# Kernel optimization log

Measured on AMD Instinct MI355X. Metric: run time of the kernel, lower is better.

The kernel has to match this reference:

```python
import jax, jax.numpy as jnp
import numpy as np

# norse default LIFParameters
DT = 1e-3
TAU_SYN_INV = 200.0
TAU_MEM_INV = 100.0
V_LEAK = 0.0
V_TH = 1.0
V_RESET = 0.0


def heaviside(x):
    return (x > 0).astype(x.dtype)


def setup_inputs() -> dict:
    key = jax.random.key(0)
    ks = jax.random.split(key, 5)
    T, B, I, H, O = 14, 4096, 2048, 1024, 128
    x = (jax.random.uniform(ks[0], (T, B, I), dtype=jnp.float32) < 0.2).astype(jnp.float32)  # spike train
    w_in = jax.random.normal(ks[1], (H, I), dtype=jnp.float32) * (1.0 / np.sqrt(I))
    w_rec = jax.random.normal(ks[2], (H, H), dtype=jnp.float32) * (1.0 / np.sqrt(H))
    out_w = jax.random.normal(ks[3], (O, H), dtype=jnp.float32) * (1.0 / np.sqrt(H))
    out_b = jax.random.normal(ks[4], (O,), dtype=jnp.float32) * 0.01
    return {"x": x, "w_in": w_in, "w_rec": w_rec, "out_w": out_w, "out_b": out_b}


def reference(x, w_in, w_rec, out_w, out_b):
    T, B, _ = x.shape
    H = w_in.shape[0]
    z0 = jnp.zeros((B, H), dtype=x.dtype)
    v0 = jnp.full((B, H), V_LEAK, dtype=x.dtype)
    i0 = jnp.zeros((B, H), dtype=x.dtype)

    def step(carry, x_t):
        z, v, i = carry
        v_dec = v + DT * TAU_MEM_INV * ((V_LEAK - v) + i)   # membrane integration
        i_dec = i - DT * TAU_SYN_INV * i                    # synaptic decay
        z_new = heaviside(v_dec - V_TH)                     # spike
        v_new = (1.0 - z_new) * v_dec + z_new * V_RESET     # reset
        i_new = i_dec + x_t @ w_in.T + z @ w_rec.T          # input + recurrent current
        return (z_new, v_new, i_new), None

    (z_T, _, _), _ = jax.lax.scan(step, (z0, v0, i0), x)
    return z_T @ out_w.T + out_b
```

## Files before the change

kernel.cpp:

```cpp
#include <hip/hip_runtime.h>
#include <stdint.h>

#define T_STEPS 14
#define B_DIM   4096
#define I_DIM   2048
#define H_DIM   1024
#define O_DIM   128
#define K_TOT   3072
#define ZBYTES  ((size_t)B_DIM * H_DIM)

#define WSCALE_F 33554432.0f

typedef __bf16  bf16x8  __attribute__((ext_vector_type(8)));
typedef float   floatx4 __attribute__((ext_vector_type(4)));
typedef int     int4v   __attribute__((ext_vector_type(4)));
typedef int     int16v  __attribute__((ext_vector_type(16)));
typedef unsigned long long u64;

__device__ __forceinline__ uint16_t f2bf_rne(float f) {
    uint32_t u = __float_as_uint(f);
    u += 0x7fffu + ((u >> 16) & 1u);
    return (uint16_t)(u >> 16);
}
__device__ __forceinline__ float bf2f(uint16_t h) {
    return __uint_as_float(((uint32_t)h) << 16);
}

__device__ __forceinline__ void gload_lds16(const void* g, void* l) {
    __builtin_amdgcn_global_load_lds((__attribute__((address_space(1))) void*)g,
                                     (__attribute__((address_space(3))) void*)l, 16, 0, 0);
}


__global__ void split_w_kernel(const float* __restrict__ w_in, const float* __restrict__ w_rec,
                               int8_t* __restrict__ WB) {
    int idx = blockIdx.x * 256 + threadIdx.x;
    int h = idx / K_TOT;
    int k = idx - h * K_TOT;
    float w = (k < I_DIM) ? w_in[(size_t)h * I_DIM + k]
                          : w_rec[(size_t)h * H_DIM + (k - I_DIM)];
    int W  = __float2int_rn(w * WSCALE_F);
    int d0 = (int8_t)(W & 0xFF);
    int r1 = (W - d0) >> 8;
    int d1 = (int8_t)(r1 & 0xFF);
    int d2 = (r1 - d1) >> 8;
    int nt = h >> 5, n32 = h & 31;
    int ktw = k >> 7, k128 = k & 127;
    int kk = k128 >> 5, half = (k128 >> 4) & 1, j = k128 & 15;
    int lane = half * 32 + n32;
    size_t base = (size_t)(nt * 24 + ktw) * 12288 + kk * 1024 + lane * 16 + j;
    WB[base] = (int8_t)d0; WB[base + 4096] = (int8_t)d1; WB[base + 8192] = (int8_t)d2;
}

__global__ void split_ow_kernel(const float* __restrict__ out_w, uint16_t* __restrict__ OW3) {
    int idx = blockIdx.x * 256 + threadIdx.x;
    float w = out_w[idx];
    uint16_t hi = f2bf_rne(w);
    float r1 = w - bf2f(hi);
    uint16_t mid = f2bf_rne(r1);
    float r2 = r1 - bf2f(mid);
    uint16_t lo = f2bf_rne(r2);
    const size_t S = (size_t)O_DIM * H_DIM;
    OW3[idx] = hi; OW3[idx + S] = mid; OW3[idx + 2 * S] = lo;
}

__global__ void cvt_x_kernel(const float* __restrict__ x, int8_t* __restrict__ xb) {
    size_t gid = (size_t)blockIdx.x * 256 + threadIdx.x;
    int g = (int)(gid & 1023);
    size_t chunk = gid >> 10;
    int kt   = (int)(chunk & 15);
    int mIdx = (int)((chunk >> 4) & 31);
    int t    = (int)(chunk >> 9);
    int group = g >> 8, kk = (g >> 6) & 3, lane = g & 63;
    int half = lane >> 5, row32 = lane & 31;
    int b = mIdx * 128 + group * 32 + row32;
    int k = kt * 128 + kk * 32 + half * 16;
    const float4* src = (const float4*)(x + ((size_t)t * B_DIM + b) * I_DIM + k);
    union { int8_t bytes[16]; int4v v; } u;
#pragma unroll
    for (int q = 0; q < 4; ++q) {
        float4 f = src[q];
        u.bytes[q * 4 + 0] = (int8_t)(f.x > 0.5f);
        u.bytes[q * 4 + 1] = (int8_t)(f.y > 0.5f);
        u.bytes[q * 4 + 2] = (int8_t)(f.z > 0.5f);
        u.bytes[q * 4 + 3] = (int8_t)(f.w > 0.5f);
    }
    ((int4v*)xb)[gid] = u.v;
}

__global__ void zero_cnt_kernel(uint32_t* __restrict__ cnt) {
    __hip_atomic_store(&cnt[blockIdx.x * 256 + threadIdx.x], 0u,
                       __ATOMIC_RELAXED, __HIP_MEMORY_SCOPE_AGENT);
}

__device__ __forceinline__ void loadA(const int8_t* __restrict__ aP, int4v (&a)[4]) {
    a[0] = *(const int4v*)(aP);
    a[1] = *(const int4v*)(aP + 1024);
    a[2] = *(const int4v*)(aP + 2048);
    a[3] = *(const int4v*)(aP + 3072);
}

__device__ __forceinline__ void stage_b0(const int8_t* __restrict__ bChunk0,
                                         int8_t* sB0, int wave, int lane) {
    gload_lds16(bChunk0 + (size_t)wave * 1024 + lane * 16,       sB0 + wave * 1024);
    gload_lds16(bChunk0 + (size_t)(4 + wave) * 1024 + lane * 16, sB0 + (4 + wave) * 1024);
    gload_lds16(bChunk0 + (size_t)(8 + wave) * 1024 + lane * 16, sB0 + (8 + wave) * 1024);
}

__device__ __forceinline__ void lif_iter_p(const int8_t* __restrict__ aPn,
                                           const int8_t* __restrict__ bPn,
                                           const int8_t* cur, int8_t* nxt,
                                           int4v (&aC)[4], int4v (&aN)[4],
                                           int wave, int lane, bool stage_next,
                                           int16v (&acc)[3]) {
    if (stage_next) {
        loadA(aPn, aN);
        gload_lds16(bPn + (size_t)wave * 1024 + lane * 16,       nxt + wave * 1024);
        gload_lds16(bPn + (size_t)(4 + wave) * 1024 + lane * 16, nxt + (4 + wave) * 1024);
        gload_lds16(bPn + (size_t)(8 + wave) * 1024 + lane * 16, nxt + (8 + wave) * 1024);
        __builtin_amdgcn_sched_barrier(0);
        asm volatile("s_waitcnt vmcnt(7)" ::: "memory");
    } else {
        asm volatile("s_waitcnt vmcnt(0)" ::: "memory");
    }
    __builtin_amdgcn_s_barrier();
    __builtin_amdgcn_sched_barrier(0);
#pragma unroll
    for (int kk = 0; kk < 4; ++kk) {
#pragma unroll
        for (int s = 0; s < 3; ++s) {
            int4v bF = *(const int4v*)(cur + s * 4096 + kk * 1024 + lane * 16);
            acc[s] = __builtin_amdgcn_mfma_i32_32x32x32_i8(aC[kk], bF, acc[s], 0, 0, 0);
        }
    }
    asm volatile("s_waitcnt lgkmcnt(0)" ::: "memory");
    __builtin_amdgcn_s_barrier();
}

template<int NKT>
__device__ __forceinline__ void run_phase(const int8_t* __restrict__ aW,
                                          const int8_t* __restrict__ bC,
                                          int8_t* sB0, int8_t* sB1,
                                          int4v (&aA)[4], int4v (&aB)[4],
                                          int wave, int lane, int16v (&acc)[3]) {
#pragma unroll 1
    for (int kt = 0; kt + 2 < NKT; kt += 2) {
        lif_iter_p(aW + (size_t)(kt + 1) * 16384, bC + (size_t)(kt + 1) * 12288,
                   sB0, sB1, aA, aB, wave, lane, true, acc);
        lif_iter_p(aW + (size_t)(kt + 2) * 16384, bC + (size_t)(kt + 2) * 12288,
                   sB1, sB0, aB, aA, wave, lane, true, acc);
    }
    lif_iter_p(aW + (size_t)(NKT - 1) * 16384, bC + (size_t)(NKT - 1) * 12288,
               sB0, sB1, aA, aB, wave, lane, true, acc);
    lif_iter_p(nullptr, nullptr, sB1, sB0, aB, aA, wave, lane, false, acc);
}

__launch_bounds__(256, 4)
__global__ void lif_persist_kernel(const int8_t* __restrict__ Xall,
                                   const int8_t* __restrict__ WB,
                                   int8_t* __restrict__ ZS,
                                   uint16_t* __restrict__ Zbf,
                                   uint32_t* __restrict__ cnt) {
    __shared__ int8_t sB0[12288];
    __shared__ int8_t sB1[12288];
    __shared__ int8_t sZ[4096];

    const int tid  = threadIdx.x;
    const int wave = tid >> 6, lane = tid & 63;
    const int lane32 = lane & 31, hl = lane >> 5;

    const int bid = blockIdx.x;
    const int xs = bid & 7, q = bid >> 3;
    const int mIdx = (xs & 1) * 16 + (q & 15);
    const int nt   = (xs >> 1) * 8 + (q >> 4);

    const int mBase = mIdx * 128, nBase = nt * 32;
    const int8_t* wbStrip = WB + (size_t)nt * 24 * 12288;
    const int fragOff = wave * 4096 + lane * 16;

    float vmem[16], isyn[16];
#pragma unroll
    for (int r = 0; r < 16; ++r) { vmem[r] = 0.0f; isyn[r] = 0.0f; }

    int4v aA[4], aB[4];

    stage_b0(wbStrip, sB0, wave, lane);
    loadA(Xall + (size_t)mIdx * 16 * 16384 + fragOff, aA);

    for (int t = 0; t < T_STEPS; ++t) {
        int16v acc[3] = {};

        const int8_t* XtW = Xall + (size_t)t * ((size_t)B_DIM * I_DIM)
                          + (size_t)mIdx * 16 * 16384 + fragOff;
        run_phase<16>(XtW, wbStrip, sB0, sB1, aA, aB, wave, lane, acc);

        if (t > 0) {
            const int8_t* zbChunk = wbStrip + (size_t)16 * 12288;
            stage_b0(zbChunk, sB0, wave, lane);
            if (tid == 0) {
                const uint32_t* f = cnt + ((size_t)mIdx * 13 + (t - 1)) * 32;
                while (__hip_atomic_load((uint32_t*)f, __ATOMIC_RELAXED, __HIP_MEMORY_SCOPE_AGENT) < 32u)
                    __builtin_amdgcn_s_sleep(2);
            }
            __syncthreads();
            const int8_t* zW = ZS + (size_t)(t - 1) * ZBYTES + (size_t)mIdx * 8 * 16384 + fragOff;
            loadA(zW, aA);
            run_phase<8>(zW, zbChunk, sB0, sB1, aA, aB, wave, lane, acc);
        }

        if (t + 1 < T_STEPS) {
            stage_b0(wbStrip, sB0, wave, lane);
            loadA(Xall + (size_t)(t + 1) * ((size_t)B_DIM * I_DIM)
                  + (size_t)mIdx * 16 * 16384 + fragOff, aA);
        }

#pragma unroll
        for (int r = 0; r < 16; ++r) {
#pragma clang fp contract(off)
            float cur = (float)acc[2][r] * (1.0f / 512.0f)
                      + (float)acc[1][r] * (1.0f / 131072.0f)
                      + (float)acc[0][r] * (1.0f / 33554432.0f);
            int row = (r & 3) + 8 * (r >> 2) + 4 * hl;
            float v_dec = vmem[r] + 0.1f * ((0.0f - vmem[r]) + isyn[r]);
            float i_dec = isyn[r] - 0.2f * isyn[r];
            bool z = (v_dec > 1.0f);
            vmem[r] = z ? 0.0f : v_dec;
            isyn[r] = i_dec + cur;
            if (t == T_STEPS - 1) {
                int b = mBase + wave * 32 + row;
                int h = nBase + lane32;
                Zbf[(size_t)b * H_DIM + h] = z ? (uint16_t)0x3F80 : (uint16_t)0;
            } else {
                sZ[wave * 1024 + ((lane32 >> 4) * 32 + row) * 16 + (lane32 & 15)]
                    = z ? (int8_t)1 : (int8_t)0;
            }
        }

        if (t < T_STEPS - 1) {
            __syncthreads();
            const u64* sp = (const u64*)&sZ[tid * 16];
            u64 v0 = sp[0], v1 = sp[1];
            int8_t* dst = ZS + (size_t)t * ZBYTES + ((size_t)mIdx * 8 + (nt >> 2)) * 16384
                        + (tid >> 6) * 4096 + (nt & 3) * 1024 + (tid & 63) * 16;
            __hip_atomic_store((u64*)dst,       v0, __ATOMIC_RELAXED, __HIP_MEMORY_SCOPE_AGENT);
            __hip_atomic_store((u64*)(dst + 8), v1, __ATOMIC_RELAXED, __HIP_MEMORY_SCOPE_AGENT);
            __syncthreads();
            if (tid == 0)
                __hip_atomic_fetch_add(&cnt[((size_t)mIdx * 13 + t) * 32], 1u,
                                       __ATOMIC_RELAXED, __HIP_MEMORY_SCOPE_AGENT);
        }
    }
}

__launch_bounds__(256)
__global__ void out_gemm_kernel(const uint16_t* __restrict__ Zfin,
                                const uint16_t* __restrict__ OW3,
                                const float* __restrict__ out_b,
                                float* __restrict__ out) {
    __shared__ uint16_t sA[16 * 32];
    __shared__ uint16_t sB[3][128 * 32];

    const int tid  = threadIdx.x;
    const int wave = tid >> 6, lane = tid & 63;
    const int quad = lane >> 4, col = lane & 15;

    const int mBase = blockIdx.x * 16;

    floatx4 acc[2] = {};

    const int ldRow = lane >> 2;
    const int ldCol = (lane & 3) * 8;

    for (int kt = 0; kt < H_DIM / 32; ++kt) {
        const int kb = kt * 32;
        __syncthreads();
        if (wave == 0) {
            const uint16_t* g = Zfin + (size_t)(mBase + ldRow) * H_DIM + kb + ldCol;
            gload_lds16(g, &sA[0]);
        }
#pragma unroll
        for (int s = 0; s < 3; ++s) {
            const uint16_t* wsrc = OW3 + (size_t)s * O_DIM * H_DIM;
#pragma unroll
            for (int j = 0; j < 2; ++j) {
                const int rseg = j * 4 + wave;
                const uint16_t* g = wsrc + (size_t)(rseg * 16 + ldRow) * H_DIM + kb + ldCol;
                gload_lds16(g, &sB[s][rseg * 16 * 32]);
            }
        }
        __syncthreads();

        bf16x8 aF = *reinterpret_cast<const bf16x8*>(&sA[col * 32 + quad * 8]);
#pragma unroll
        for (int s = 0; s < 3; ++s) {
#pragma unroll
            for (int ni = 0; ni < 2; ++ni) {
                int row = wave * 32 + ni * 16 + col;
                bf16x8 bF = *reinterpret_cast<const bf16x8*>(&sB[s][row * 32 + quad * 8]);
                acc[ni] = __builtin_amdgcn_mfma_f32_16x16x32_bf16(aF, bF, acc[ni], 0, 0, 0);
            }
        }
    }

    {
#pragma clang fp contract(off)
#pragma unroll
        for (int ni = 0; ni < 2; ++ni)
#pragma unroll
            for (int r = 0; r < 4; ++r) {
                int b = mBase + quad * 4 + r;
                int h = wave * 32 + ni * 16 + col;
                out[(size_t)b * O_DIM + h] = acc[ni][r] + out_b[h];
            }
    }
}

extern "C" void kernel_launch(void* const* d_in, const int* in_sizes, int n_in,
                              void* d_out, int out_size, void* d_ws, size_t ws_size,
                              hipStream_t stream) {
    const float* x     = (const float*)d_in[0];
    const float* w_in  = (const float*)d_in[1];
    const float* w_rec = (const float*)d_in[2];
    const float* out_w = (const float*)d_in[3];
    const float* out_b = (const float*)d_in[4];
    float* out = (float*)d_out;

    char* ws = (char*)d_ws;
    size_t off = 0;
    int8_t*   WB   = (int8_t*)(ws + off);   off += (size_t)3 * H_DIM * K_TOT;
    uint16_t* OW3  = (uint16_t*)(ws + off); off += (size_t)3 * O_DIM * H_DIM * 2;
    int8_t*   Xall = (int8_t*)(ws + off);   off += (size_t)T_STEPS * B_DIM * I_DIM;
    uint16_t* Zbf  = (uint16_t*)(ws + off); off += (size_t)B_DIM * H_DIM * 2;
    int8_t*   ZS   = (int8_t*)(ws + off);   off += (size_t)13 * ZBYTES;
    uint32_t* CNT  = (uint32_t*)(ws + off); off += (size_t)32 * 13 * 32 * 4;

    split_w_kernel<<<(H_DIM * K_TOT) / 256, 256, 0, stream>>>(w_in, w_rec, WB);
    split_ow_kernel<<<(O_DIM * H_DIM) / 256, 256, 0, stream>>>(out_w, OW3);
    cvt_x_kernel<<<(int)(((size_t)T_STEPS * B_DIM * I_DIM / 16) / 256), 256, 0, stream>>>(x, Xall);
    zero_cnt_kernel<<<(32 * 13 * 32) / 256, 256, 0, stream>>>(CNT);

    lif_persist_kernel<<<dim3(1024), dim3(256), 0, stream>>>(Xall, WB, ZS, Zbf, CNT);

    out_gemm_kernel<<<B_DIM / 16, 256, 0, stream>>>(Zbf, OW3, out_b, out);
}
```

Before: 1.356 ms.

## Single-buffer A fragments, issue next A loads after MFMAs, raise MFMA priority, remap blocks

Replaces the double-buffered A register fragments with a single set that is reloaded right after the MFMA block finishes, which frees registers. The wait count drops because only the B LDS copies are outstanding at the wait. MFMA sections are wrapped with s_setprio to favour matrix work. The block-to-tile mapping also changes so neighbouring blocks share different M/N strips, which alters L2 reuse. In exchange, A loads are no longer hidden behind a full iteration of compute.

```diff
diff --git a/kernel.cpp b/kernel.cpp
--- a/kernel.cpp
+++ b/kernel.cpp
@@ -107,32 +107,35 @@
     gload_lds16(bChunk0 + (size_t)(8 + wave) * 1024 + lane * 16, sB0 + (8 + wave) * 1024);
 }
 
-__device__ __forceinline__ void lif_iter_p(const int8_t* __restrict__ aPn,
-                                           const int8_t* __restrict__ bPn,
-                                           const int8_t* cur, int8_t* nxt,
-                                           int4v (&aC)[4], int4v (&aN)[4],
-                                           int wave, int lane, bool stage_next,
-                                           int16v (&acc)[3]) {
+__device__ __forceinline__ void lif_iter(const int8_t* __restrict__ aPn,
+                                         const int8_t* __restrict__ bPn,
+                                         const int8_t* cur, int8_t* nxt,
+                                         int4v (&aA)[4],
+                                         int wave, int lane, bool stage_next,
+                                         int16v (&acc)[3]) {
     if (stage_next) {
-        loadA(aPn, aN);
         gload_lds16(bPn + (size_t)wave * 1024 + lane * 16,       nxt + wave * 1024);
         gload_lds16(bPn + (size_t)(4 + wave) * 1024 + lane * 16, nxt + (4 + wave) * 1024);
         gload_lds16(bPn + (size_t)(8 + wave) * 1024 + lane * 16, nxt + (8 + wave) * 1024);
         __builtin_amdgcn_sched_barrier(0);
-        asm volatile("s_waitcnt vmcnt(7)" ::: "memory");
+        asm volatile("s_waitcnt vmcnt(3)" ::: "memory");
     } else {
         asm volatile("s_waitcnt vmcnt(0)" ::: "memory");
     }
     __builtin_amdgcn_s_barrier();
     __builtin_amdgcn_sched_barrier(0);
+    __builtin_amdgcn_s_setprio(1);
 #pragma unroll
     for (int kk = 0; kk < 4; ++kk) {
 #pragma unroll
         for (int s = 0; s < 3; ++s) {
             int4v bF = *(const int4v*)(cur + s * 4096 + kk * 1024 + lane * 16);
-            acc[s] = __builtin_amdgcn_mfma_i32_32x32x32_i8(aC[kk], bF, acc[s], 0, 0, 0);
-        }
-    }
+            acc[s] = __builtin_amdgcn_mfma_i32_32x32x32_i8(aA[kk], bF, acc[s], 0, 0, 0);
+        }
+    }
+    __builtin_amdgcn_s_setprio(0);
+    __builtin_amdgcn_sched_barrier(0);
+    if (aPn) loadA(aPn, aA);
     asm volatile("s_waitcnt lgkmcnt(0)" ::: "memory");
     __builtin_amdgcn_s_barrier();
 }
@@ -141,18 +144,18 @@
 __device__ __forceinline__ void run_phase(const int8_t* __restrict__ aW,
                                           const int8_t* __restrict__ bC,
                                           int8_t* sB0, int8_t* sB1,
-                                          int4v (&aA)[4], int4v (&aB)[4],
+                                          int4v (&aA)[4],
                                           int wave, int lane, int16v (&acc)[3]) {
 #pragma unroll 1
     for (int kt = 0; kt + 2 < NKT; kt += 2) {
-        lif_iter_p(aW + (size_t)(kt + 1) * 16384, bC + (size_t)(kt + 1) * 12288,
-                   sB0, sB1, aA, aB, wave, lane, true, acc);
-        lif_iter_p(aW + (size_t)(kt + 2) * 16384, bC + (size_t)(kt + 2) * 12288,
-                   sB1, sB0, aB, aA, wave, lane, true, acc);
-    }
-    lif_iter_p(aW + (size_t)(NKT - 1) * 16384, bC + (size_t)(NKT - 1) * 12288,
-               sB0, sB1, aA, aB, wave, lane, true, acc);
-    lif_iter_p(nullptr, nullptr, sB1, sB0, aB, aA, wave, lane, false, acc);
+        lif_iter(aW + (size_t)(kt + 1) * 16384, bC + (size_t)(kt + 1) * 12288,
+                 sB0, sB1, aA, wave, lane, true, acc);
+        lif_iter(aW + (size_t)(kt + 2) * 16384, bC + (size_t)(kt + 2) * 12288,
+                 sB1, sB0, aA, wave, lane, true, acc);
+    }
+    lif_iter(aW + (size_t)(NKT - 1) * 16384, bC + (size_t)(NKT - 1) * 12288,
+             sB0, sB1, aA, wave, lane, true, acc);
+    lif_iter(nullptr, nullptr, sB1, sB0, aA, wave, lane, false, acc);
 }
 
 __launch_bounds__(256, 4)
@@ -171,8 +174,8 @@
 
     const int bid = blockIdx.x;
     const int xs = bid & 7, q = bid >> 3;
-    const int mIdx = (xs & 1) * 16 + (q & 15);
-    const int nt   = (xs >> 1) * 8 + (q >> 4);
+    const int mIdx = xs * 4 + (q & 3);
+    const int nt   = q >> 2;
 
     const int mBase = mIdx * 128, nBase = nt * 32;
     const int8_t* wbStrip = WB + (size_t)nt * 24 * 12288;
@@ -182,7 +185,7 @@
 #pragma unroll
     for (int r = 0; r < 16; ++r) { vmem[r] = 0.0f; isyn[r] = 0.0f; }
 
-    int4v aA[4], aB[4];
+    int4v aA[4];
 
     stage_b0(wbStrip, sB0, wave, lane);
     loadA(Xall + (size_t)mIdx * 16 * 16384 + fragOff, aA);
@@ -192,7 +195,7 @@
 
         const int8_t* XtW = Xall + (size_t)t * ((size_t)B_DIM * I_DIM)
                           + (size_t)mIdx * 16 * 16384 + fragOff;
-        run_phase<16>(XtW, wbStrip, sB0, sB1, aA, aB, wave, lane, acc);
+        run_phase<16>(XtW, wbStrip, sB0, sB1, aA, wave, lane, acc);
 
         if (t > 0) {
             const int8_t* zbChunk = wbStrip + (size_t)16 * 12288;
@@ -205,7 +208,7 @@
             __syncthreads();
             const int8_t* zW = ZS + (size_t)(t - 1) * ZBYTES + (size_t)mIdx * 8 * 16384 + fragOff;
             loadA(zW, aA);
-            run_phase<8>(zW, zbChunk, sB0, sB1, aA, aB, wave, lane, acc);
+            run_phase<8>(zW, zbChunk, sB0, sB1, aA, wave, lane, acc);
         }
 
         if (t + 1 < T_STEPS) {
```

Result: faster. 1.295 ms (-4.4%).
